# Optimization experiments

Hardware: AMD Instinct MI355X
Metric: run time of the kernel (lower is better)

Reference implementation:

```python
import jax, jax.numpy as jnp
import numpy as np

N_NODES = 100000
N_EDGES = 500000
H = 128
EPS = 1e-5


def _mlp(x, W1, b1, W2, b2, W3, b3, g, beta):
    # 3-layer MLP (ReLU) + final LayerNorm, matching build_mlp(..., lay_norm=True, n_layers=3)
    h = jax.nn.relu(x @ W1 + b1)
    h = jax.nn.relu(h @ W2 + b2)
    h = h @ W3 + b3
    mu = jnp.mean(h, axis=-1, keepdims=True)
    var = jnp.var(h, axis=-1, keepdims=True)
    return (h - mu) * jax.lax.rsqrt(var + EPS) * g + beta


def setup_inputs() -> dict:
    key = jax.random.key(0)
    ks = jax.random.split(key, 20)
    s = lambda fan_in: 1.0 / np.sqrt(fan_in)
    inp = {
        "x": jax.random.normal(ks[0], (N_NODES, H), dtype=jnp.float32),
        "edge_attr": jax.random.normal(ks[1], (N_EDGES, H), dtype=jnp.float32),
        "edge_index": jax.random.randint(ks[2], (2, N_EDGES), 0, N_NODES, dtype=jnp.int64),
        # Edge MLP: in = 3H
        "eW1": jax.random.normal(ks[3], (3 * H, H), dtype=jnp.float32) * s(3 * H),
        "eb1": jnp.zeros((H,), jnp.float32),
        "eW2": jax.random.normal(ks[4], (H, H), dtype=jnp.float32) * s(H),
        "eb2": jnp.zeros((H,), jnp.float32),
        "eW3": jax.random.normal(ks[5], (H, H), dtype=jnp.float32) * s(H),
        "eb3": jnp.zeros((H,), jnp.float32),
        "eg": jnp.ones((H,), jnp.float32),
        "ebeta": jnp.zeros((H,), jnp.float32),
        # Node MLP: in = 2H
        "nW1": jax.random.normal(ks[6], (2 * H, H), dtype=jnp.float32) * s(2 * H),
        "nb1": jnp.zeros((H,), jnp.float32),
        "nW2": jax.random.normal(ks[7], (H, H), dtype=jnp.float32) * s(H),
        "nb2": jnp.zeros((H,), jnp.float32),
        "nW3": jax.random.normal(ks[8], (H, H), dtype=jnp.float32) * s(H),
        "nb3": jnp.zeros((H,), jnp.float32),
        "ng": jnp.ones((H,), jnp.float32),
        "nbeta": jnp.zeros((H,), jnp.float32),
    }
    return inp


def reference(x, edge_attr, edge_index,
              eW1, eb1, eW2, eb2, eW3, eb3, eg, ebeta,
              nW1, nb1, nW2, nb2, nW3, nb3, ng, nbeta):
    senders = edge_index[0]
    receivers = edge_index[1]
    # EdgeBlock: gather src/dst node feats, concat with edge feats, MLP (3H -> H)
    e_in = jnp.concatenate([x[senders], x[receivers], edge_attr], axis=-1)
    e_new = _mlp(e_in, eW1, eb1, eW2, eb2, eW3, eb3, eg, ebeta)
    # NodeBlock: scatter-sum edge messages to receiver nodes, concat with node feats, MLP (2H -> H)
    agg = jax.ops.segment_sum(e_new, receivers, num_segments=N_NODES)
    n_in = jnp.concatenate([x, agg], axis=-1)
    x_new = _mlp(n_in, nW1, nb1, nW2, nb2, nW3, nb3, ng, nbeta)
    # Residual connections
    return (x + x_new, edge_attr + e_new)
```

## Files before the change

kernel.cpp:

```cpp
#include <hip/hip_runtime.h>
#include <hip/hip_bf16.h>

#define N_NODES 100000
#define N_EDGES 500000
#define H 128
#define EPS 1e-5f

typedef __attribute__((ext_vector_type(8))) short bf16x8;
typedef __attribute__((ext_vector_type(4))) float f32x4;

__device__ __forceinline__ unsigned short f2bf(float f) {
  unsigned int u = __builtin_bit_cast(unsigned int, f);
  u += 0x7FFFu + ((u >> 16) & 1u);
  return (unsigned short)(u >> 16);
}

__device__ __forceinline__ int swz(int r, int k) {
  return r * 128 + (k ^ ((r & 7) << 3));
}

union PK8 { unsigned short u[8]; uint4 q; };

#define GLDS16(g, l)                                                        \
  __builtin_amdgcn_global_load_lds(                                         \
      (const __attribute__((address_space(1))) void*)(g),                   \
      (__attribute__((address_space(3))) void*)(l), 16, 0, 0)

__device__ __forceinline__ void stage_a_half(unsigned short* Abuf, int r, int k0,
                                             const float* src) {
  #pragma unroll
  for (int j = 0; j < 8; ++j) {
    PK8 pk;
    if (src) {
      float4 v0 = *(const float4*)(src + j * 8);
      float4 v1 = *(const float4*)(src + j * 8 + 4);
      pk.u[0] = f2bf(v0.x); pk.u[1] = f2bf(v0.y);
      pk.u[2] = f2bf(v0.z); pk.u[3] = f2bf(v0.w);
      pk.u[4] = f2bf(v1.x); pk.u[5] = f2bf(v1.y);
      pk.u[6] = f2bf(v1.z); pk.u[7] = f2bf(v1.w);
    } else {
      #pragma unroll
      for (int q = 0; q < 8; ++q) pk.u[q] = 0;
    }
    *(uint4*)&Abuf[swz(r, k0 + j * 8)] = pk.q;
  }
}

__device__ __forceinline__ void stage_w_async(unsigned short* Wbuf,
                                              const unsigned short* img) {
  const int t = threadIdx.x;
  #pragma unroll
  for (int j = 0; j < 8; ++j) {
    const int byteoff = j * 4096 + t * 16;
    GLDS16((const char*)img + byteoff, (char*)Wbuf + byteoff);
  }
}

__device__ __forceinline__ void gemm128(const unsigned short* Abuf,
                                        const unsigned short* Wbuf,
                                        int row_base, int m0, int kq,
                                        f32x4 acc[2][8]) {
  #pragma unroll
  for (int kk = 0; kk < 4; ++kk) {
    const int k0 = kk * 32 + kq * 8;
    bf16x8 a0 = *(const bf16x8*)&Abuf[swz(row_base + m0, k0)];
    bf16x8 a1 = *(const bf16x8*)&Abuf[swz(row_base + 16 + m0, k0)];
    #pragma unroll
    for (int tc = 0; tc < 8; ++tc) {
      bf16x8 b = *(const bf16x8*)&Wbuf[swz(tc * 16 + m0, k0)];
      acc[0][tc] = __builtin_amdgcn_mfma_f32_16x16x32_bf16(a0, b, acc[0][tc], 0, 0, 0);
      acc[1][tc] = __builtin_amdgcn_mfma_f32_16x16x32_bf16(a1, b, acc[1][tc], 0, 0, 0);
    }
  }
}

__device__ __forceinline__ void write_hidden_relu(unsigned short* Abuf, f32x4 acc[2][8],
                                                  const float* __restrict__ bias,
                                                  int row_base, int m0, int kq) {
  #pragma unroll
  for (int tc = 0; tc < 8; ++tc) {
    const int col = tc * 16 + m0;
    const float b = bias[col];
    #pragma unroll
    for (int tr = 0; tr < 2; ++tr)
      #pragma unroll
      for (int i = 0; i < 4; ++i)
        Abuf[swz(row_base + tr * 16 + kq * 4 + i, col)] =
            f2bf(fmaxf(acc[tr][tc][i] + b, 0.0f));
  }
}

__device__ __forceinline__ void zero_acc(f32x4 acc[2][8]) {
  #pragma unroll
  for (int a = 0; a < 2; ++a)
    #pragma unroll
    for (int b = 0; b < 8; ++b)
      acc[a][b] = (f32x4){0.f, 0.f, 0.f, 0.f};
}

__device__ __forceinline__ void ln_stats(const f32x4 acc[2][8], float mu[2][4],
                                         float rv[2][4]) {
  #pragma unroll
  for (int tr = 0; tr < 2; ++tr) {
    float s[4] = {0, 0, 0, 0}, ss[4] = {0, 0, 0, 0};
    #pragma unroll
    for (int tc = 0; tc < 8; ++tc)
      #pragma unroll
      for (int i = 0; i < 4; ++i) {
        const float v = acc[tr][tc][i];
        s[i] += v;
        ss[i] += v * v;
      }
    #pragma unroll
    for (int off = 1; off < 16; off <<= 1) {
      #pragma unroll
      for (int i = 0; i < 4; ++i) {
        s[i] += __shfl_xor(s[i], off);
        ss[i] += __shfl_xor(ss[i], off);
      }
    }
    #pragma unroll
    for (int i = 0; i < 4; ++i) {
      const float m = s[i] * (1.0f / 128.0f);
      const float var = ss[i] * (1.0f / 128.0f) - m * m;
      mu[tr][i] = m;
      rv[tr][i] = rsqrtf(var + EPS);
    }
  }
}


__global__ void hist_kernel(const int* __restrict__ ridx, unsigned* __restrict__ cnt) {
  const int e = blockIdx.x * 256 + threadIdx.x;
  if (e < N_EDGES) atomicAdd(&cnt[ridx[e]], 1u);
}

__global__ void scan1_kernel(const unsigned* __restrict__ cnt,
                             unsigned* __restrict__ offs,
                             unsigned* __restrict__ part) {
  __shared__ unsigned sh[256];
  const int t = threadIdx.x;
  const int base = blockIdx.x * 1024 + t * 4;
  unsigned v[4];
  #pragma unroll
  for (int i = 0; i < 4; ++i) v[i] = (base + i < N_NODES) ? cnt[base + i] : 0u;
  unsigned pre[4];
  pre[0] = 0; pre[1] = v[0]; pre[2] = v[0] + v[1]; pre[3] = pre[2] + v[2];
  const unsigned tot = pre[3] + v[3];
  sh[t] = tot;
  __syncthreads();
  for (int d = 1; d < 256; d <<= 1) {
    const unsigned u_ = (t >= d) ? sh[t - d] : 0u;
    __syncthreads();
    sh[t] += u_;
    __syncthreads();
  }
  const unsigned excl = sh[t] - tot;
  #pragma unroll
  for (int i = 0; i < 4; ++i)
    if (base + i < N_NODES) offs[base + i] = excl + pre[i];
  if (t == 255) part[blockIdx.x] = sh[255];
}

__global__ void scan2_kernel(unsigned* __restrict__ part, int n) {
  __shared__ unsigned sh[128];
  const int t = threadIdx.x;
  const unsigned v = (t < n) ? part[t] : 0u;
  sh[t] = v;
  __syncthreads();
  for (int d = 1; d < 128; d <<= 1) {
    const unsigned u_ = (t >= d) ? sh[t - d] : 0u;
    __syncthreads();
    sh[t] += u_;
    __syncthreads();
  }
  if (t < n) part[t] = sh[t] - v;
}

__global__ void scan3_kernel(unsigned* __restrict__ offs,
                             const unsigned* __restrict__ part,
                             unsigned* __restrict__ cursor) {
  const int i = blockIdx.x * 256 + threadIdx.x;
  if (i < N_NODES) {
    const unsigned o = offs[i] + part[i >> 10];
    offs[i] = o;
    cursor[i] = o;
  }
  if (i == 0) offs[N_NODES] = N_EDGES;
}

__global__ void scatter_kernel(const int* __restrict__ ridx,
                               unsigned* __restrict__ cursor,
                               unsigned* __restrict__ eord) {
  const int e = blockIdx.x * 256 + threadIdx.x;
  if (e < N_EDGES) {
    const unsigned p = atomicAdd(&cursor[ridx[e]], 1u);
    eord[p] = (unsigned)e;
  }
}


struct WSrc { const float* p[9]; };

__global__ void wprep_kernel(WSrc wsrc, unsigned short* __restrict__ wimg) {
  const int id = blockIdx.x * 256 + threadIdx.x;
  const int m = id >> 14;
  const int r = id & 16383;
  const int n = r & 127;
  const int k = r >> 7;
  wimg[m * 16384 + swz(n, k)] = f2bf(wsrc.p[m][k * 128 + n]);
}


__global__ __launch_bounds__(256, 2) void edge_kernel(
    const float* __restrict__ x, const float* __restrict__ edge_attr,
    const int* __restrict__ eidx, const unsigned short* __restrict__ wimg,
    const float* __restrict__ eb1, const float* __restrict__ eb2,
    const float* __restrict__ eb3,
    const float* __restrict__ eg, const float* __restrict__ ebeta,
    float* __restrict__ out_e, unsigned short* __restrict__ enew) {
  __shared__ unsigned short Abuf[128 * 128];
  __shared__ unsigned short Wbuf[128 * 128];

  const int t = threadIdx.x;
  const int lane = t & 63;
  const int wave = t >> 6;
  const int row_base = wave * 32;
  const int m0 = lane & 15;
  const int kq = lane >> 4;
  const long e0 = (long)blockIdx.x * 128;
  const int* sidx = eidx;
  const int* ridx = eidx + N_EDGES;

  const int sr = t >> 1;
  const int sk0 = (t & 1) * 64;
  const long se = e0 + sr;
  const bool svalid = (se < N_EDGES);

  f32x4 acc[2][8];
  zero_acc(acc);

  for (int p = 0; p < 3; ++p) {
    __syncthreads();
    const float* src = nullptr;
    if (svalid) {
      if (p == 0)      src = x + (long)sidx[se] * H + sk0;
      else if (p == 1) src = x + (long)ridx[se] * H + sk0;
      else             src = edge_attr + se * (long)H + sk0;
    }
    stage_a_half(Abuf, sr, sk0, src);
    stage_w_async(Wbuf, wimg + (long)p * 16384);
    __syncthreads();
    gemm128(Abuf, Wbuf, row_base, m0, kq, acc);
  }

  __syncthreads();
  write_hidden_relu(Abuf, acc, eb1, row_base, m0, kq);
  stage_w_async(Wbuf, wimg + 3L * 16384);
  zero_acc(acc);
  __syncthreads();
  gemm128(Abuf, Wbuf, row_base, m0, kq, acc);

  __syncthreads();
  write_hidden_relu(Abuf, acc, eb2, row_base, m0, kq);
  stage_w_async(Wbuf, wimg + 4L * 16384);
  zero_acc(acc);
  __syncthreads();
  gemm128(Abuf, Wbuf, row_base, m0, kq, acc);

  float gm[8], bt[8];
  #pragma unroll
  for (int tc = 0; tc < 8; ++tc) {
    const int col = tc * 16 + m0;
    const float b3 = eb3[col];
    gm[tc] = eg[col];
    bt[tc] = ebeta[col];
    #pragma unroll
    for (int tr = 0; tr < 2; ++tr)
      #pragma unroll
      for (int i = 0; i < 4; ++i)
        acc[tr][tc][i] += b3;
  }
  float mu[2][4], rv[2][4];
  ln_stats(acc, mu, rv);

  #pragma unroll
  for (int tr = 0; tr < 2; ++tr)
    #pragma unroll
    for (int i = 0; i < 4; ++i) {
      const int row = row_base + tr * 16 + kq * 4 + i;
      const long e = e0 + row;
      if (e < N_EDGES) {
        const float m_ = mu[tr][i], r_ = rv[tr][i];
        const float* ea = edge_attr + e * (long)H;
        float* oe = out_e + e * (long)H;
        unsigned short* en = enew + e * (long)H;
        #pragma unroll
        for (int tc = 0; tc < 8; ++tc) {
          const int col = tc * 16 + m0;
          const float y = (acc[tr][tc][i] - m_) * r_ * gm[tc] + bt[tc];
          oe[col] = ea[col] + y;
          en[col] = f2bf(y);
        }
      }
    }
}

__global__ __launch_bounds__(256, 2) void node_kernel(
    const float* __restrict__ x, const unsigned short* __restrict__ enew,
    const unsigned* __restrict__ offs, const unsigned* __restrict__ eord,
    const unsigned short* __restrict__ wimg,
    const float* __restrict__ nb1, const float* __restrict__ nb2,
    const float* __restrict__ nb3,
    const float* __restrict__ ng, const float* __restrict__ nbeta,
    float* __restrict__ out_x) {
  __shared__ unsigned short Abuf[128 * 128];
  __shared__ unsigned short Wbuf[128 * 128];

  const int t = threadIdx.x;
  const int lane = t & 63;
  const int wave = t >> 6;
  const int row_base = wave * 32;
  const int m0 = lane & 15;
  const int kq = lane >> 4;
  const long n0 = (long)blockIdx.x * 128;

  const int sr = t >> 1;
  const int sk0 = (t & 1) * 64;
  const long sn = n0 + sr;
  const bool svalid = (sn < N_NODES);

  f32x4 acc[2][8];
  zero_acc(acc);

  stage_a_half(Abuf, sr, sk0, svalid ? x + sn * (long)H + sk0 : nullptr);
  stage_w_async(Wbuf, wimg + 5L * 16384);
  __syncthreads();
  gemm128(Abuf, Wbuf, row_base, m0, kq, acc);

  __syncthreads();
  {
    float av[64];
    #pragma unroll
    for (int i = 0; i < 64; ++i) av[i] = 0.f;
    if (svalid) {
      const unsigned o0 = offs[sn], o1 = offs[sn + 1];
      for (unsigned u_ = o0; u_ < o1; ++u_) {
        const unsigned short* er = enew + (long)eord[u_] * H + sk0;
        #pragma unroll
        for (int j = 0; j < 8; ++j) {
          uint4 q = *(const uint4*)(er + j * 8);
          const unsigned short* pu = (const unsigned short*)&q;
          #pragma unroll
          for (int c = 0; c < 8; ++c)
            av[j * 8 + c] += __builtin_bit_cast(float, (unsigned)pu[c] << 16);
        }
      }
    }
    #pragma unroll
    for (int j = 0; j < 8; ++j) {
      PK8 pk;
      #pragma unroll
      for (int c = 0; c < 8; ++c) pk.u[c] = f2bf(av[j * 8 + c]);
      *(uint4*)&Abuf[swz(sr, sk0 + j * 8)] = pk.q;
    }
  }
  stage_w_async(Wbuf, wimg + 6L * 16384);
  __syncthreads();
  gemm128(Abuf, Wbuf, row_base, m0, kq, acc);

  __syncthreads();
  write_hidden_relu(Abuf, acc, nb1, row_base, m0, kq);
  stage_w_async(Wbuf, wimg + 7L * 16384);
  zero_acc(acc);
  __syncthreads();
  gemm128(Abuf, Wbuf, row_base, m0, kq, acc);

  __syncthreads();
  write_hidden_relu(Abuf, acc, nb2, row_base, m0, kq);
  stage_w_async(Wbuf, wimg + 8L * 16384);
  zero_acc(acc);
  __syncthreads();
  gemm128(Abuf, Wbuf, row_base, m0, kq, acc);

  float gm[8], bt[8];
  #pragma unroll
  for (int tc = 0; tc < 8; ++tc) {
    const int col = tc * 16 + m0;
    const float b3 = nb3[col];
    gm[tc] = ng[col];
    bt[tc] = nbeta[col];
    #pragma unroll
    for (int tr = 0; tr < 2; ++tr)
      #pragma unroll
      for (int i = 0; i < 4; ++i)
        acc[tr][tc][i] += b3;
  }
  float mu[2][4], rv[2][4];
  ln_stats(acc, mu, rv);

  #pragma unroll
  for (int tr = 0; tr < 2; ++tr)
    #pragma unroll
    for (int i = 0; i < 4; ++i) {
      const int row = row_base + tr * 16 + kq * 4 + i;
      const long n = n0 + row;
      if (n < N_NODES) {
        const float m_ = mu[tr][i], r_ = rv[tr][i];
        const float* xr = x + n * (long)H;
        float* ox = out_x + n * (long)H;
        #pragma unroll
        for (int tc = 0; tc < 8; ++tc) {
          const int col = tc * 16 + m0;
          const float y = (acc[tr][tc][i] - m_) * r_ * gm[tc] + bt[tc];
          ox[col] = xr[col] + y;
        }
      }
    }
}

extern "C" void kernel_launch(void* const* d_in, const int* in_sizes, int n_in,
                              void* d_out, int out_size, void* d_ws, size_t ws_size,
                              hipStream_t stream) {
  (void)in_sizes; (void)n_in; (void)out_size; (void)ws_size;
  const float* x         = (const float*)d_in[0];
  const float* edge_attr = (const float*)d_in[1];
  const int*   eidx      = (const int*)d_in[2];
  const float* eW1 = (const float*)d_in[3];
  const float* eb1 = (const float*)d_in[4];
  const float* eW2 = (const float*)d_in[5];
  const float* eb2 = (const float*)d_in[6];
  const float* eW3 = (const float*)d_in[7];
  const float* eb3 = (const float*)d_in[8];
  const float* eg  = (const float*)d_in[9];
  const float* ebt = (const float*)d_in[10];
  const float* nW1 = (const float*)d_in[11];
  const float* nb1 = (const float*)d_in[12];
  const float* nW2 = (const float*)d_in[13];
  const float* nb2 = (const float*)d_in[14];
  const float* nW3 = (const float*)d_in[15];
  const float* nb3 = (const float*)d_in[16];
  const float* ng  = (const float*)d_in[17];
  const float* nbt = (const float*)d_in[18];

  float* out_x = (float*)d_out;
  float* out_e = (float*)d_out + (size_t)N_NODES * H;

  char* w = (char*)d_ws;
  unsigned short* enew = (unsigned short*)(w + 0);
  unsigned short* wimg = (unsigned short*)(w + 128000000);
  unsigned* offs   = (unsigned*)(w + 128327680);
  unsigned* cnt    = (unsigned*)(w + 128727808);
  unsigned* cursor = (unsigned*)(w + 129127936);
  unsigned* part   = (unsigned*)(w + 129528064);
  unsigned* eord   = (unsigned*)(w + 129529088);

  const int* ridx = eidx + N_EDGES;

  hipMemsetAsync(cnt, 0, (size_t)N_NODES * sizeof(unsigned), stream);

  WSrc wsrc;
  wsrc.p[0] = eW1;
  wsrc.p[1] = eW1 + 16384;
  wsrc.p[2] = eW1 + 32768;
  wsrc.p[3] = eW2;
  wsrc.p[4] = eW3;
  wsrc.p[5] = nW1;
  wsrc.p[6] = nW1 + 16384;
  wsrc.p[7] = nW2;
  wsrc.p[8] = nW3;
  wprep_kernel<<<576, 256, 0, stream>>>(wsrc, wimg);

  hist_kernel<<<(N_EDGES + 255) / 256, 256, 0, stream>>>(ridx, cnt);
  scan1_kernel<<<(N_NODES + 1023) / 1024, 256, 0, stream>>>(cnt, offs, part);
  scan2_kernel<<<1, 128, 0, stream>>>(part, (N_NODES + 1023) / 1024);
  scan3_kernel<<<(N_NODES + 255) / 256, 256, 0, stream>>>(offs, part, cursor);
  scatter_kernel<<<(N_EDGES + 255) / 256, 256, 0, stream>>>(ridx, cursor, eord);

  const int eblocks = (N_EDGES + 127) / 128;
  const int nblocks = (N_NODES + 127) / 128;
  edge_kernel<<<eblocks, 256, 0, stream>>>(x, edge_attr, eidx, wimg, eb1, eb2, eb3,
                                           eg, ebt, out_e, enew);
  node_kernel<<<nblocks, 256, 0, stream>>>(x, enew, offs, eord, wimg, nb1, nb2, nb3,
                                           ng, nbt, out_x);
}
```

Before: 447.4 us.

## Pre-convert x to bf16, gather via async LDS loads, read weights from global

Adds a pass that converts x to bf16 once, so the edge and node kernels gather bf16 node rows with global_load_lds straight into swizzled shared memory instead of loading fp32 and converting per edge. Weight tiles are no longer staged in LDS: the GEMM reads B fragments directly from a row-major bf16 weight image in global memory (L2-resident), which halves LDS use and raises the occupancy hint from 2 to 4 blocks per CU. Epilogues now stage the normalized output through LDS as bf16 and write coalesced 128-bit rows, at the cost that out_e and out_x residuals add a bf16-rounded y instead of the full fp32 value.

Result: slower. 958.3 us (+114.2%).

```diff
diff --git a/kernel.cpp b/kernel.cpp
--- a/kernel.cpp
+++ b/kernel.cpp
@@ -14,6 +14,9 @@
   u += 0x7FFFu + ((u >> 16) & 1u);
   return (unsigned short)(u >> 16);
 }
+__device__ __forceinline__ float bf2f(unsigned short u) {
+  return __builtin_bit_cast(float, (unsigned)u << 16);
+}
 
 __device__ __forceinline__ int swz(int r, int k) {
   return r * 128 + (k ^ ((r & 7) << 3));
@@ -25,6 +28,7 @@
   __builtin_amdgcn_global_load_lds(                                         \
       (const __attribute__((address_space(1))) void*)(g),                   \
       (__attribute__((address_space(3))) void*)(l), 16, 0, 0)
+
 
 __device__ __forceinline__ void stage_a_half(unsigned short* Abuf, int r, int k0,
                                              const float* src) {
@@ -46,20 +50,40 @@
   }
 }
 
-__device__ __forceinline__ void stage_w_async(unsigned short* Wbuf,
-                                              const unsigned short* img) {
+__device__ __forceinline__ void stage_gather(const unsigned short* xb,
+                                             const int* __restrict__ idx, long e0,
+                                             unsigned short* Abuf) {
   const int t = threadIdx.x;
+  const int c = t & 15;
   #pragma unroll
   for (int j = 0; j < 8; ++j) {
-    const int byteoff = j * 4096 + t * 16;
-    GLDS16((const char*)img + byteoff, (char*)Wbuf + byteoff);
-  }
-}
-
-__device__ __forceinline__ void gemm128(const unsigned short* Abuf,
-                                        const unsigned short* Wbuf,
-                                        int row_base, int m0, int kq,
-                                        f32x4 acc[2][8]) {
+    const int r = j * 16 + (t >> 4);
+    long e = e0 + r;
+    if (e > N_EDGES - 1) e = N_EDGES - 1;
+    const long node = idx[e];
+    const unsigned short* src = xb + node * H + ((c ^ (r & 7)) * 8);
+    GLDS16(src, (char*)Abuf + j * 4096 + t * 16);
+  }
+}
+
+__device__ __forceinline__ void stage_seq(const unsigned short* xb, long n0,
+                                          unsigned short* Abuf) {
+  const int t = threadIdx.x;
+  const int c = t & 15;
+  #pragma unroll
+  for (int j = 0; j < 8; ++j) {
+    const int r = j * 16 + (t >> 4);
+    long n = n0 + r;
+    if (n > N_NODES - 1) n = N_NODES - 1;
+    const unsigned short* src = xb + n * H + ((c ^ (r & 7)) * 8);
+    GLDS16(src, (char*)Abuf + j * 4096 + t * 16);
+  }
+}
+
+__device__ __forceinline__ void gemm128_gw(const unsigned short* Abuf,
+                                           const unsigned short* __restrict__ wt,
+                                           int row_base, int m0, int kq,
+                                           f32x4 acc[2][8]) {
   #pragma unroll
   for (int kk = 0; kk < 4; ++kk) {
     const int k0 = kk * 32 + kq * 8;
@@ -67,7 +91,7 @@
     bf16x8 a1 = *(const bf16x8*)&Abuf[swz(row_base + 16 + m0, k0)];
     #pragma unroll
     for (int tc = 0; tc < 8; ++tc) {
-      bf16x8 b = *(const bf16x8*)&Wbuf[swz(tc * 16 + m0, k0)];
+      bf16x8 b = *(const bf16x8*)&wt[(tc * 16 + m0) * H + k0];
       acc[0][tc] = __builtin_amdgcn_mfma_f32_16x16x32_bf16(a0, b, acc[0][tc], 0, 0, 0);
       acc[1][tc] = __builtin_amdgcn_mfma_f32_16x16x32_bf16(a1, b, acc[1][tc], 0, 0, 0);
     }
@@ -127,6 +151,34 @@
       rv[tr][i] = rsqrtf(var + EPS);
     }
   }
+}
+
+
+__global__ void xprep_kernel(const float* __restrict__ x,
+                             unsigned short* __restrict__ xb) {
+  const long i = (long)blockIdx.x * 256 + threadIdx.x;
+  const long base = i * 8;
+  if (base < (long)N_NODES * H) {
+    float4 v0 = *(const float4*)(x + base);
+    float4 v1 = *(const float4*)(x + base + 4);
+    PK8 pk;
+    pk.u[0] = f2bf(v0.x); pk.u[1] = f2bf(v0.y);
+    pk.u[2] = f2bf(v0.z); pk.u[3] = f2bf(v0.w);
+    pk.u[4] = f2bf(v1.x); pk.u[5] = f2bf(v1.y);
+    pk.u[6] = f2bf(v1.z); pk.u[7] = f2bf(v1.w);
+    *(uint4*)(xb + base) = pk.q;
+  }
+}
+
+struct WSrc { const float* p[9]; };
+
+__global__ void wprep_kernel(WSrc wsrc, unsigned short* __restrict__ wimg) {
+  const int id = blockIdx.x * 256 + threadIdx.x;
+  const int m = id >> 14;
+  const int r = id & 16383;
+  const int n = r & 127;
+  const int k = r >> 7;
+  wimg[m * 16384 + n * 128 + k] = f2bf(wsrc.p[m][k * 128 + n]);
 }
 
 
@@ -200,27 +252,14 @@
 }
 
 
-struct WSrc { const float* p[9]; };
-
-__global__ void wprep_kernel(WSrc wsrc, unsigned short* __restrict__ wimg) {
-  const int id = blockIdx.x * 256 + threadIdx.x;
-  const int m = id >> 14;
-  const int r = id & 16383;
-  const int n = r & 127;
-  const int k = r >> 7;
-  wimg[m * 16384 + swz(n, k)] = f2bf(wsrc.p[m][k * 128 + n]);
-}
-
-
-__global__ __launch_bounds__(256, 2) void edge_kernel(
-    const float* __restrict__ x, const float* __restrict__ edge_attr,
+__global__ __launch_bounds__(256, 4) void edge_kernel(
+    const unsigned short* __restrict__ xb, const float* __restrict__ edge_attr,
     const int* __restrict__ eidx, const unsigned short* __restrict__ wimg,
     const float* __restrict__ eb1, const float* __restrict__ eb2,
     const float* __restrict__ eb3,
     const float* __restrict__ eg, const float* __restrict__ ebeta,
     float* __restrict__ out_e, unsigned short* __restrict__ enew) {
   __shared__ unsigned short Abuf[128 * 128];
-  __shared__ unsigned short Wbuf[128 * 128];
 
   const int t = threadIdx.x;
   const int lane = t & 63;
@@ -234,39 +273,39 @@
 
   const int sr = t >> 1;
   const int sk0 = (t & 1) * 64;
-  const long se = e0 + sr;
-  const bool svalid = (se < N_EDGES);
 
   f32x4 acc[2][8];
   zero_acc(acc);
 
-  for (int p = 0; p < 3; ++p) {
-    __syncthreads();
-    const float* src = nullptr;
-    if (svalid) {
-      if (p == 0)      src = x + (long)sidx[se] * H + sk0;
-      else if (p == 1) src = x + (long)ridx[se] * H + sk0;
-      else             src = edge_attr + se * (long)H + sk0;
-    }
-    stage_a_half(Abuf, sr, sk0, src);
-    stage_w_async(Wbuf, wimg + (long)p * 16384);
-    __syncthreads();
-    gemm128(Abuf, Wbuf, row_base, m0, kq, acc);
-  }
+  stage_gather(xb, sidx, e0, Abuf);
+  __syncthreads();
+  gemm128_gw(Abuf, wimg + 0L * 16384, row_base, m0, kq, acc);
+  __syncthreads();
+
+  stage_gather(xb, ridx, e0, Abuf);
+  __syncthreads();
+  gemm128_gw(Abuf, wimg + 1L * 16384, row_base, m0, kq, acc);
+  __syncthreads();
+
+  {
+    const long se = e0 + sr;
+    stage_a_half(Abuf, sr, sk0,
+                 (se < N_EDGES) ? edge_attr + se * (long)H + sk0 : nullptr);
+  }
+  __syncthreads();
+  gemm128_gw(Abuf, wimg + 2L * 16384, row_base, m0, kq, acc);
 
   __syncthreads();
   write_hidden_relu(Abuf, acc, eb1, row_base, m0, kq);
-  stage_w_async(Wbuf, wimg + 3L * 16384);
   zero_acc(acc);
   __syncthreads();
-  gemm128(Abuf, Wbuf, row_base, m0, kq, acc);
+  gemm128_gw(Abuf, wimg + 3L * 16384, row_base, m0, kq, acc);
 
   __syncthreads();
   write_hidden_relu(Abuf, acc, eb2, row_base, m0, kq);
-  stage_w_async(Wbuf, wimg + 4L * 16384);
   zero_acc(acc);
   __syncthreads();
-  gemm128(Abuf, Wbuf, row_base, m0, kq, acc);
+  gemm128_gw(Abuf, wimg + 4L * 16384, row_base, m0, kq, acc);
 
   float gm[8], bt[8];
   #pragma unroll
@@ -284,30 +323,47 @@
   float mu[2][4], rv[2][4];
   ln_stats(acc, mu, rv);
 
-  #pragma unroll
-  for (int tr = 0; tr < 2; ++tr)
-    #pragma unroll
-    for (int i = 0; i < 4; ++i) {
-      const int row = row_base + tr * 16 + kq * 4 + i;
-      const long e = e0 + row;
-      if (e < N_EDGES) {
-        const float m_ = mu[tr][i], r_ = rv[tr][i];
-        const float* ea = edge_attr + e * (long)H;
-        float* oe = out_e + e * (long)H;
-        unsigned short* en = enew + e * (long)H;
-        #pragma unroll
-        for (int tc = 0; tc < 8; ++tc) {
-          const int col = tc * 16 + m0;
-          const float y = (acc[tr][tc][i] - m_) * r_ * gm[tc] + bt[tc];
-          oe[col] = ea[col] + y;
-          en[col] = f2bf(y);
-        }
+  __syncthreads();
+  #pragma unroll
+  for (int tc = 0; tc < 8; ++tc) {
+    const int col = tc * 16 + m0;
+    #pragma unroll
+    for (int tr = 0; tr < 2; ++tr)
+      #pragma unroll
+      for (int i = 0; i < 4; ++i) {
+        const float y = (acc[tr][tc][i] - mu[tr][i]) * rv[tr][i] * gm[tc] + bt[tc];
+        Abuf[swz(row_base + tr * 16 + kq * 4 + i, col)] = f2bf(y);
       }
-    }
+  }
+  __syncthreads();
+  {
+    const long e = e0 + sr;
+    if (e < N_EDGES) {
+      const float* ea = edge_attr + e * (long)H + sk0;
+      float* oe = out_e + e * (long)H + sk0;
+      unsigned short* en = enew + e * (long)H + sk0;
+      #pragma unroll
+      for (int c2 = 0; c2 < 8; ++c2) {
+        uint4 q = *(const uint4*)&Abuf[swz(sr, sk0 + c2 * 8)];
+        *(uint4*)(en + c2 * 8) = q;
+        const unsigned short* pu = (const unsigned short*)&q;
+        float4 a0 = *(const float4*)(ea + c2 * 8);
+        float4 a1 = *(const float4*)(ea + c2 * 8 + 4);
+        float4 o0, o1;
+        o0.x = a0.x + bf2f(pu[0]); o0.y = a0.y + bf2f(pu[1]);
+        o0.z = a0.z + bf2f(pu[2]); o0.w = a0.w + bf2f(pu[3]);
+        o1.x = a1.x + bf2f(pu[4]); o1.y = a1.y + bf2f(pu[5]);
+        o1.z = a1.z + bf2f(pu[6]); o1.w = a1.w + bf2f(pu[7]);
+        *(float4*)(oe + c2 * 8) = o0;
+        *(float4*)(oe + c2 * 8 + 4) = o1;
+      }
+    }
+  }
 }
 
 __global__ __launch_bounds__(256, 2) void node_kernel(
-    const float* __restrict__ x, const unsigned short* __restrict__ enew,
+    const unsigned short* __restrict__ xb, const float* __restrict__ x,
+    const unsigned short* __restrict__ enew,
     const unsigned* __restrict__ offs, const unsigned* __restrict__ eord,
     const unsigned short* __restrict__ wimg,
     const float* __restrict__ nb1, const float* __restrict__ nb2,
@@ -315,7 +371,6 @@
     const float* __restrict__ ng, const float* __restrict__ nbeta,
     float* __restrict__ out_x) {
   __shared__ unsigned short Abuf[128 * 128];
-  __shared__ unsigned short Wbuf[128 * 128];
 
   const int t = threadIdx.x;
   const int lane = t & 63;
@@ -333,12 +388,11 @@
   f32x4 acc[2][8];
   zero_acc(acc);
 
-  stage_a_half(Abuf, sr, sk0, svalid ? x + sn * (long)H + sk0 : nullptr);
-  stage_w_async(Wbuf, wimg + 5L * 16384);
-  __syncthreads();
-  gemm128(Abuf, Wbuf, row_base, m0, kq, acc);
-
-  __syncthreads();
+  stage_seq(xb, n0, Abuf);
+  __syncthreads();
+  gemm128_gw(Abuf, wimg + 5L * 16384, row_base, m0, kq, acc);
+  __syncthreads();
+
   {
     float av[64];
     #pragma unroll
@@ -353,7 +407,7 @@
           const unsigned short* pu = (const unsigned short*)&q;
           #pragma unroll
           for (int c = 0; c < 8; ++c)
-            av[j * 8 + c] += __builtin_bit_cast(float, (unsigned)pu[c] << 16);
+            av[j * 8 + c] += bf2f(pu[c]);
         }
       }
     }
@@ -365,23 +419,20 @@
       *(uint4*)&Abuf[swz(sr, sk0 + j * 8)] = pk.q;
     }
   }
-  stage_w_async(Wbuf, wimg + 6L * 16384);
-  __syncthreads();
-  gemm128(Abuf, Wbuf, row_base, m0, kq, acc);
+  __syncthreads();
+  gemm128_gw(Abuf, wimg + 6L * 16384, row_base, m0, kq, acc);
 
   __syncthreads();
   write_hidden_relu(Abuf, acc, nb1, row_base, m0, kq);
-  stage_w_async(Wbuf, wimg + 7L * 16384);
   zero_acc(acc);
   __syncthreads();
-  gemm128(Abuf, Wbuf, row_base, m0, kq, acc);
+  gemm128_gw(Abuf, wimg + 7L * 16384, row_base, m0, kq, acc);
 
   __syncthreads();
   write_hidden_relu(Abuf, acc, nb2, row_base, m0, kq);
-  stage_w_async(Wbuf, wimg + 8L * 16384);
   zero_acc(acc);
   __syncthreads();
-  gemm128(Abuf, Wbuf, row_base, m0, kq, acc);
+  gemm128_gw(Abuf, wimg + 8L * 16384, row_base, m0, kq, acc);
 
   float gm[8], bt[8];
   #pragma unroll
@@ -399,24 +450,37 @@
   float mu[2][4], rv[2][4];
   ln_stats(acc, mu, rv);
 
-  #pragma unroll
-  for (int tr = 0; tr < 2; ++tr)
-    #pragma unroll
-    for (int i = 0; i < 4; ++i) {
-      const int row = row_base + tr * 16 + kq * 4 + i;
-      const long n = n0 + row;
-      if (n < N_NODES) {
-        const float m_ = mu[tr][i], r_ = rv[tr][i];
-        const float* xr = x + n * (long)H;
-        float* ox = out_x + n * (long)H;
-        #pragma unroll
-        for (int tc = 0; tc < 8; ++tc) {
-          const int col = tc * 16 + m0;
-          const float y = (acc[tr][tc][i] - m_) * r_ * gm[tc] + bt[tc];
-          ox[col] = xr[col] + y;
-        }
+  __syncthreads();
+  #pragma unroll
+  for (int tc = 0; tc < 8; ++tc) {
+    const int col = tc * 16 + m0;
+    #pragma unroll
+    for (int tr = 0; tr < 2; ++tr)
+      #pragma unroll
+      for (int i = 0; i < 4; ++i) {
+        const float y = (acc[tr][tc][i] - mu[tr][i]) * rv[tr][i] * gm[tc] + bt[tc];
+        Abuf[swz(row_base + tr * 16 + kq * 4 + i, col)] = f2bf(y);
       }
-    }
+  }
+  __syncthreads();
+  if (svalid) {
+    const float* xr = x + sn * (long)H + sk0;
+    float* ox = out_x + sn * (long)H + sk0;
+    #pragma unroll
+    for (int c2 = 0; c2 < 8; ++c2) {
+      uint4 q = *(const uint4*)&Abuf[swz(sr, sk0 + c2 * 8)];
+      const unsigned short* pu = (const unsigned short*)&q;
+      float4 a0 = *(const float4*)(xr + c2 * 8);
+      float4 a1 = *(const float4*)(xr + c2 * 8 + 4);
+      float4 o0, o1;
+      o0.x = a0.x + bf2f(pu[0]); o0.y = a0.y + bf2f(pu[1]);
+      o0.z = a0.z + bf2f(pu[2]); o0.w = a0.w + bf2f(pu[3]);
+      o1.x = a1.x + bf2f(pu[4]); o1.y = a1.y + bf2f(pu[5]);
+      o1.z = a1.z + bf2f(pu[6]); o1.w = a1.w + bf2f(pu[7]);
+      *(float4*)(ox + c2 * 8) = o0;
+      *(float4*)(ox + c2 * 8 + 4) = o1;
+    }
+  }
 }
 
 extern "C" void kernel_launch(void* const* d_in, const int* in_sizes, int n_in,
@@ -448,12 +512,13 @@
 
   char* w = (char*)d_ws;
   unsigned short* enew = (unsigned short*)(w + 0);
-  unsigned short* wimg = (unsigned short*)(w + 128000000);
-  unsigned* offs   = (unsigned*)(w + 128327680);
-  unsigned* cnt    = (unsigned*)(w + 128727808);
-  unsigned* cursor = (unsigned*)(w + 129127936);
-  unsigned* part   = (unsigned*)(w + 129528064);
-  unsigned* eord   = (unsigned*)(w + 129529088);
+  unsigned short* xb   = (unsigned short*)(w + 128000000);
+  unsigned short* wimg = (unsigned short*)(w + 153600000);
+  unsigned* offs   = (unsigned*)(w + 153894912);
+  unsigned* cnt    = (unsigned*)(w + 154295040);
+  unsigned* cursor = (unsigned*)(w + 154695168);
+  unsigned* part   = (unsigned*)(w + 155095296);
+  unsigned* eord   = (unsigned*)(w + 155096320);
 
   const int* ridx = eidx + N_EDGES;
 
@@ -469,6 +534,8 @@
   wsrc.p[6] = nW1 + 16384;
   wsrc.p[7] = nW2;
   wsrc.p[8] = nW3;
+
+  xprep_kernel<<<(N_NODES * H / 8 + 255) / 256, 256, 0, stream>>>(x, xb);
   wprep_kernel<<<576, 256, 0, stream>>>(wsrc, wimg);
 
   hist_kernel<<<(N_EDGES + 255) / 256, 256, 0, stream>>>(ridx, cnt);
@@ -479,8 +546,8 @@
 
   const int eblocks = (N_EDGES + 127) / 128;
   const int nblocks = (N_NODES + 127) / 128;
-  edge_kernel<<<eblocks, 256, 0, stream>>>(x, edge_attr, eidx, wimg, eb1, eb2, eb3,
+  edge_kernel<<<eblocks, 256, 0, stream>>>(xb, edge_attr, eidx, wimg, eb1, eb2, eb3,
                                            eg, ebt, out_e, enew);
-  node_kernel<<<nblocks, 256, 0, stream>>>(x, enew, offs, eord, wimg, nb1, nb2, nb3,
-                                           ng, nbt, out_x);
-}
+  node_kernel<<<nblocks, 256, 0, stream>>>(xb, x, enew, offs, eord, wimg,
+                                           nb1, nb2, nb3, ng, nbt, out_x);
+}
```
